# Kernel tuning notes

Hardware: AMD Instinct MI355X
Metric: run time of the kernel (lower is better)

The kernel has to match this reference:

```python
import jax, jax.numpy as jnp
import numpy as np
import math

NLAT, NLON, LMAX, MMAX = 128, 256, 50, 50
M = NLAT * NLON  # = 2*NLAT^2 grid points, matches torch meshgrid(arange(nlat), arange(-nlat,nlat))

def _grid_np():
    gx, gy = np.meshgrid(np.arange(NLAT), np.arange(-NLAT, NLAT), indexing='ij')
    g = np.stack([gx.ravel(), gy.ravel()], -1).astype(np.float32)
    return g / NLAT * np.pi  # (M, 2)

def _cc_weights(n):
    # Clenshaw-Curtis quadrature nodes theta_j = pi*j/(n-1) and weights on [-1,1]
    N = n - 1
    theta = np.pi * np.arange(n) / N
    k = np.arange(1, N // 2 + 1)
    b = np.where(2 * k == N, 1.0, 2.0)
    S = (b / (4.0 * k ** 2 - 1.0) * np.cos(2.0 * np.outer(theta, k))).sum(-1)
    w = (2.0 / N) * (1.0 - S)
    w[0] *= 0.5
    w[-1] *= 0.5
    return theta, w

def _legendre(lmax, mmax, theta):
    # orthonormal (4pi-normalized) associated Legendre P_l^m(cos theta), Condon-Shortley phase
    x, s = np.cos(theta), np.sin(theta)
    P = np.zeros((mmax, lmax, theta.shape[0]))
    P[0, 0] = math.sqrt(1.0 / (4.0 * math.pi))
    pmm = P[0, 0].copy()
    for m in range(1, mmax):
        pmm = -math.sqrt((2 * m + 1) / (2.0 * m)) * s * pmm
        P[m, m] = pmm
    for m in range(mmax):
        if m + 1 < lmax:
            P[m, m + 1] = math.sqrt(2 * m + 3.0) * x * P[m, m]
        for l in range(m + 2, lmax):
            a = math.sqrt((4.0 * l * l - 1.0) / (l * l - m * m))
            bb = math.sqrt(((l - 1.0) ** 2 - m * m) / (4.0 * (l - 1.0) ** 2 - 1.0))
            P[m, l] = a * (x * P[m, l - 1] - bb * P[m, l - 2])
    return P

_theta_q, _wq = _cc_weights(NLAT)
_SHT_W = jnp.asarray((_legendre(LMAX, MMAX, _theta_q) * _wq).astype(np.float32))  # (mmax, lmax, nlat)
_GRID = jnp.asarray(_grid_np())  # (M, 2)

def setup_inputs() -> dict:
    key = jax.random.key(0)
    target = jax.random.normal(key, (2, 2048, 3), dtype=jnp.float32)
    return {"target": target}

def reference(target):
    B, N, _ = target.shape
    # to_spherical: rho=(B,N) features, sph=(phi, theta)-pi shift on theta -> (B,N,2)
    rho = jnp.linalg.norm(target, axis=-1)
    phi = jnp.arctan2(target[..., 1], target[..., 0])
    theta = jnp.arccos(target[..., 2] / rho)
    sph = jnp.stack([phi, theta - jnp.pi], axis=-1)  # (B, N, 2)
    # squared distances grid(M,2) vs sph(B,N,2) -> (B,M,N) via gram trick (no (B,M,N,2) temp)
    s2 = jnp.sum(sph * sph, -1)                 # (B, N)
    g2 = jnp.sum(_GRID * _GRID, -1)             # (M,)
    cross = jnp.einsum('md,bnd->bmn', _GRID, sph)
    D2 = jax.lax.stop_gradient(s2[:, None, :] + g2[None, :, None] - 2.0 * cross)
    _, idx = jax.lax.top_k(-D2, 3)              # (B, M, 3), 3-NN targets per grid point, ascending dist
    bidx = jnp.arange(B)[:, None, None]
    tmp = sph[bidx, idx]                        # (B, M, 3, 2)
    dist = jnp.sqrt(jnp.sum((tmp - _GRID[None, :, None, :]) ** 2, -1))  # (B, M, 3)
    w = dist / jnp.sum(dist, -1, keepdims=True)
    # three_interpolate: weighted combine of rho at 3 NNs -> (B, M)
    interp = jnp.sum(rho[bidx, idx] * w, -1)
    f = interp.reshape(B, NLAT, NLON)
    # RealSHT (equiangular grid): forward-normalized rfft over lon, then Legendre contraction over lat
    F = (2.0 * jnp.pi) * jnp.fft.rfft(f, axis=-1) / NLON  # (B, nlat, nlon//2+1) complex
    coeff_re = jnp.einsum('bkm,mlk->blm', jnp.real(F[..., :MMAX]), _SHT_W)  # (B, lmax, mmax)
    return coeff_re
```

## Files before the change

kernel.cpp:

```cpp
#include <hip/hip_runtime.h>
#include <math.h>
#include <stdint.h>

#define NLAT 128
#define NLON 256
#define LMAX 50
#define MMAX 50
#define MGRID (NLAT*NLON)
#define BATCH 2
#define NPTS 2048
#define NBKT 64
#define PI_F 3.14159265358979323846f

typedef float v2f __attribute__((ext_vector_type(2)));

__device__ __forceinline__ uint32_t umin32(uint32_t a, uint32_t b) { return a < b ? a : b; }
__device__ __forceinline__ uint32_t umax32(uint32_t a, uint32_t b) { return a > b ? a : b; }

__global__ __launch_bounds__(512, 2)
void k_nn(const float* __restrict__ target, float* __restrict__ f) {
    __shared__ __attribute__((aligned(16))) float2 s_all[NPTS + 8];
    __shared__ float    s_rall[NPTS + 8];
    __shared__ uint32_t s_keys[8*64*3];
    __shared__ int      cnt[NBKT], start[NBKT + 1], cur[NBKT];
    __shared__ int      s_win[2];
    int b = blockIdx.x >> 8;
    int j = blockIdx.x & 255;
    int tid = threadIdx.x;
    const float* tg = target + b * NPTS * 3;

    if (tid < NBKT) cnt[tid] = 0;
    __syncthreads();
    float ph[4], py[4], rh[4]; int bk[4];
    #pragma unroll
    for (int c = 0; c < 4; ++c) {
        int p = tid + c * 512;
        float x = tg[p*3], y = tg[p*3+1], z = tg[p*3+2];
        float r = sqrtf(fmaf(x, x, fmaf(y, y, z*z)));
        float cc = fminf(1.f, fmaxf(-1.f, z / r));
        float pyv = acosf(cc) - PI_F;
        ph[c] = atan2f(y, x); py[c] = pyv; rh[c] = r;
        int bb = (int)floorf((pyv + PI_F) * ((float)NBKT / PI_F));
        bk[c] = min(NBKT-1, max(0, bb));
        atomicAdd(&cnt[bk[c]], 1);
    }
    __syncthreads();

    if (tid < 64) {
        int v = cnt[tid];
        int cv = v;
        #pragma unroll
        for (int sh = 1; sh < 64; sh <<= 1) {
            int t = __shfl_up(v, sh);
            if (tid >= sh) v += t;
        }
        start[tid + 1] = v;
        cur[tid] = v - cv;
        if (tid == 0) start[0] = 0;
    }
    __syncthreads();

    #pragma unroll
    for (int c = 0; c < 4; ++c) {
        int pos = atomicAdd(&cur[bk[c]], 1);
        s_all[pos]  = make_float2(ph[c], py[c]);
        s_rall[pos] = rh[c];
    }
    if (tid < 8) {
        s_all[NPTS + tid] = make_float2(1e15f, 1e15f);
        s_rall[NPTS + tid] = 0.f;
    }
    float gy = (float)(j - 128) * (PI_F / 128.0f);
    int c0 = (int)floorf((gy + PI_F) * ((float)NBKT / PI_F));
    c0 = min(NBKT-1, max(0, c0));
    if (tid < 64) {
        int t = tid;
        int lo_t = max(0, c0 - 5 - t), hi_t = min(NBKT-1, c0 + 5 + t);
        int cw_t = start[hi_t+1] - start[lo_t];
        unsigned long long ok =
            __ballot(cw_t >= 192 || (lo_t == 0 && hi_t == NBKT-1));
        int t0 = __ffsll((unsigned long long)ok) - 1;
        if (tid == 0) {
            s_win[0] = max(0, c0 - 5 - t0);
            s_win[1] = min(NBKT-1, c0 + 5 + t0);
        }
    }
    __syncthreads();

    int lo = s_win[0], hi = s_win[1];
    int off = start[lo] & ~1;
    int cw  = start[hi+1] - off;
    int q = ((cw + 3) / 4 + 1) & ~1;
    int lane = tid & 63;
    int wv   = tid >> 6;
    int part = wv & 3;
    int lat  = lane + ((wv >> 2) << 6);
    float gx = (float)lat * (PI_F / 128.0f);
    v2f gx2 = {gx, gx}, gy2 = {gy, gy};
    uint32_t k0 = ~0u, k1 = ~0u, k2 = ~0u;
    uint32_t nb = (uint32_t)(part * q);
    const float4* p4 = (const float4*)(s_all + off + part * q);
    int iters = q >> 1;
    #pragma unroll 4
    for (int i = 0; i < iters; ++i) {
        float4 Q = p4[i];
        v2f px = {Q.x, Q.z}, pyy = {Q.y, Q.w};
        v2f dp = gx2 - px, dt = gy2 - pyy;
        v2f d = dp * dp;
        d = dt * dt + d;
        uint32_t key0 = (__float_as_uint(d.x) & 0xFFFFF800u) | (nb + 2u*i);
        uint32_t key1 = (__float_as_uint(d.y) & 0xFFFFF800u) | (nb + 2u*i + 1u);
        uint32_t t1;
        t1 = umin32(umax32(key0, k0), k1);
        k2 = umin32(umax32(key0, k1), k2);
        k0 = umin32(key0, k0); k1 = t1;
        t1 = umin32(umax32(key1, k0), k1);
        k2 = umin32(umax32(key1, k1), k2);
        k0 = umin32(key1, k0); k1 = t1;
    }
    s_keys[(wv*64 + lane)*3 + 0] = k0;
    s_keys[(wv*64 + lane)*3 + 1] = k1;
    s_keys[(wv*64 + lane)*3 + 2] = k2;
    __syncthreads();

    if (tid < 128) {
        int lane2 = tid & 63;
        int half  = tid >> 6;
        uint32_t m0 = ~0u, m1 = ~0u, m2 = ~0u;
        #pragma unroll
        for (int w = half*4; w < half*4 + 4; ++w) {
            #pragma unroll
            for (int s = 0; s < 3; ++s) {
                uint32_t key = s_keys[(w*64 + lane2)*3 + s];
                uint32_t t1 = umin32(umax32(key, m0), m1);
                m2 = umin32(umax32(key, m1), m2);
                m0 = umin32(key, m0); m1 = t1;
            }
        }
        int i0 = off + (int)(m0 & 2047);
        int i1 = off + (int)(m1 & 2047);
        int i2 = off + (int)(m2 & 2047);
        int lat2 = lane2 + (half << 6);
        float gxs = (float)lat2 * (PI_F / 128.0f);
        float2 p0 = s_all[i0], p1 = s_all[i1], p2 = s_all[i2];
        float e, r0, r1, r2;
        e = gxs - p0.x; r0 = e*e; e = gy - p0.y; r0 = sqrtf(fmaf(e, e, r0));
        e = gxs - p1.x; r1 = e*e; e = gy - p1.y; r1 = sqrtf(fmaf(e, e, r1));
        e = gxs - p2.x; r2 = e*e; e = gy - p2.y; r2 = sqrtf(fmaf(e, e, r2));
        float sum = r0 + r1 + r2;
        float interp = (s_rall[i0]*r0 + s_rall[i1]*r1 + s_rall[i2]*r2) / sum;
        f[b * MGRID + lat2 * NLON + j] = interp;
    }
}

__global__ __launch_bounds__(512)
void k_fftsht(const float* __restrict__ f, float* __restrict__ out) {
    __shared__ float Wl[LMAX*129];
    __shared__ float red[NLAT*5];
    __shared__ float sFre[NLAT];
    __shared__ float cred[256];
    __shared__ float s_a[LMAX], s_bb[LMAX], s_w[NLAT];
    __shared__ float s_cm;
    int b = blockIdx.x / MMAX;
    int m = blockIdx.x % MMAX;
    int tid = threadIdx.x;

    if (tid < 64) {
        int i = tid;
        float v = (i >= 1 && i <= m)
                  ? 0.5f * __log2f((2.f*i + 1.f) / (2.f*i)) : 0.f;
        #pragma unroll
        for (int sh = 1; sh < 64; sh <<= 1) v += __shfl_xor(v, sh);
        if (i == 0) s_cm = ((m & 1) ? -1.f : 1.f) * exp2f(v);
    } else if (tid < 128) {
        int l = tid - 64;
        if (l < LMAX) {
            float fl = (float)l, fm2 = (float)(m*m);
            s_a[l]  = sqrtf((4.f*fl*fl - 1.f) / fmaxf(fl*fl - fm2, 0.25f));
            float flm1 = fl - 1.f;
            s_bb[l] = sqrtf(fmaxf(flm1*flm1 - fm2, 0.f) /
                            fmaxf(4.f*flm1*flm1 - 1.f, 0.25f));
        }
    } else if (tid < 256) {
        int k = tid - 128;
        float theta = (PI_F * (float)k) / 127.0f;
        float S = 0.0f;
        for (int kk = 1; kk <= 63; ++kk)
            S += 2.0f / (4.0f*kk*kk - 1.0f) * __cosf(2.0f * theta * (float)kk);
        float w = (2.0f/127.0f) * (1.0f - S);
        if (k == 0 || k == NLAT-1) w *= 0.5f;
        s_w[k] = w;
    }

    {
        int k = tid >> 2, g = tid & 3;
        const float4* fb4 = (const float4*)(f + b * MGRID);
        float p = 0.0f;
        int a = (m * 64 * g) & 255;
        #pragma unroll
        for (int i = 0; i < 16; ++i) {
            float4 v = fb4[k * 64 + g * 16 + i];
            p = fmaf(v.x, __cosf((float)a * (2.0f*PI_F/256.0f)), p); a = (a + m) & 255;
            p = fmaf(v.y, __cosf((float)a * (2.0f*PI_F/256.0f)), p); a = (a + m) & 255;
            p = fmaf(v.z, __cosf((float)a * (2.0f*PI_F/256.0f)), p); a = (a + m) & 255;
            p = fmaf(v.w, __cosf((float)a * (2.0f*PI_F/256.0f)), p); a = (a + m) & 255;
        }
        red[k * 5 + g] = p;
    }
    __syncthreads();

    if (tid < NLAT) {
        int k = tid;
        float srow = red[k*5] + red[k*5+1] + red[k*5+2] + red[k*5+3];
        sFre[k] = srow * (2.0f * PI_F / 256.0f);

        float theta = (PI_F * (float)k) / 127.0f;
        float x = __cosf(theta), sn = __sinf(theta);
        float w = s_w[k];
        float pmm;
        if (m == 0) pmm = 0.28209479177f;
        else {
            float mag = exp2f((float)m * __log2f(fabsf(sn)));
            float sg  = (sn < 0.f && (m & 1)) ? -1.f : 1.f;
            pmm = 0.28209479177f * s_cm * mag * sg;
        }
        for (int l = 0; l < m; ++l) Wl[l*129 + k] = 0.0f;
        float Plm2 = pmm;
        Wl[m*129 + k] = Plm2 * w;
        if (m + 1 < LMAX) {
            float Plm1 = sqrtf(2.0f*m + 3.0f) * x * pmm;
            Wl[(m+1)*129 + k] = Plm1 * w;
            for (int l = m + 2; l < LMAX; ++l) {
                float P = s_a[l] * fmaf(-s_bb[l], Plm2, x * Plm1);
                Wl[l*129 + k] = P * w;
                Plm2 = Plm1; Plm1 = P;
            }
        }
    }
    __syncthreads();

    float acc = 0.0f;
    if (tid < 200) {
        int l = tid >> 2, kq = tid & 3;
        #pragma unroll 8
        for (int i = 0; i < 32; ++i)
            acc = fmaf(Wl[l*129 + kq*32 + i], sFre[kq*32 + i], acc);
    }
    if (tid < 256) cred[tid] = acc;
    __syncthreads();
    if (tid < LMAX)
        out[(b*LMAX + tid)*MMAX + m] =
            cred[4*tid] + cred[4*tid+1] + cred[4*tid+2] + cred[4*tid+3];
}

extern "C" void kernel_launch(void* const* d_in, const int* in_sizes, int n_in,
                              void* d_out, int out_size, void* d_ws, size_t ws_size,
                              hipStream_t stream) {
    const float* target = (const float*)d_in[0];
    float* out = (float*)d_out;
    float* f   = (float*)d_ws;

    k_nn<<<BATCH*NLON, 512, 0, stream>>>(target, f);
    k_fftsht<<<BATCH*MMAX, 512, 0, stream>>>(f, out);
}
```

Baseline: 74.92 us.

## Hoist per-batch sorting and Legendre weight tables into a separate prep kernel

```diff
diff --git a/kernel.cpp b/kernel.cpp
--- a/kernel.cpp
+++ b/kernel.cpp
@@ -10,6 +10,7 @@
 #define BATCH 2
 #define NPTS 2048
 #define NBKT 64
+#define NSRT 2056
 #define PI_F 3.14159265358979323846f
 
 typedef float v2f __attribute__((ext_vector_type(2)));
@@ -17,66 +18,154 @@
 __device__ __forceinline__ uint32_t umin32(uint32_t a, uint32_t b) { return a < b ? a : b; }
 __device__ __forceinline__ uint32_t umax32(uint32_t a, uint32_t b) { return a > b ? a : b; }
 
+#define WS_F    0
+#define WS_SXY  65536
+#define WS_SR   (WS_SXY + BATCH*NSRT*2)
+#define WS_BST  (WS_SR + BATCH*NSRT)
+#define WS_WG   78080
+#define WS_CT   (WS_WG + MMAX*LMAX*NLAT)
+
+__global__ __launch_bounds__(512)
+void k_prep(const float* __restrict__ target, float* __restrict__ ws) {
+    __shared__ __attribute__((aligned(16))) float2 s_all[NSRT];
+    __shared__ float    s_rall[NSRT];
+    __shared__ int      cnt[NBKT], start[NBKT + 1], cur[NBKT];
+    __shared__ float    s_a[LMAX], s_bb[LMAX], s_w[NLAT];
+    __shared__ float    s_cm;
+    int blk = blockIdx.x;
+    int tid = threadIdx.x;
+
+    if (blk < BATCH) {
+        const float* tg = target + blk * NPTS * 3;
+        if (tid < NBKT) cnt[tid] = 0;
+        __syncthreads();
+        float ph[4], py[4], rh[4]; int bk[4];
+        #pragma unroll
+        for (int c = 0; c < 4; ++c) {
+            int p = tid + c * 512;
+            float x = tg[p*3], y = tg[p*3+1], z = tg[p*3+2];
+            float r = sqrtf(fmaf(x, x, fmaf(y, y, z*z)));
+            float cc = fminf(1.f, fmaxf(-1.f, z / r));
+            float pyv = acosf(cc) - PI_F;
+            ph[c] = atan2f(y, x); py[c] = pyv; rh[c] = r;
+            int bb = (int)floorf((pyv + PI_F) * ((float)NBKT / PI_F));
+            bk[c] = min(NBKT-1, max(0, bb));
+            atomicAdd(&cnt[bk[c]], 1);
+        }
+        __syncthreads();
+        if (tid < 64) {
+            int v = cnt[tid];
+            int cv = v;
+            #pragma unroll
+            for (int sh = 1; sh < 64; sh <<= 1) {
+                int t = __shfl_up(v, sh);
+                if (tid >= sh) v += t;
+            }
+            start[tid + 1] = v;
+            cur[tid] = v - cv;
+            if (tid == 0) start[0] = 0;
+        }
+        __syncthreads();
+        #pragma unroll
+        for (int c = 0; c < 4; ++c) {
+            int pos = atomicAdd(&cur[bk[c]], 1);
+            s_all[pos]  = make_float2(ph[c], py[c]);
+            s_rall[pos] = rh[c];
+        }
+        if (tid < 8) {
+            s_all[NPTS + tid] = make_float2(1e15f, 1e15f);
+            s_rall[NPTS + tid] = 0.f;
+        }
+        __syncthreads();
+        float2* gxy = (float2*)(ws + WS_SXY) + blk * NSRT;
+        float*  gr  = ws + WS_SR + blk * NSRT;
+        int*    bst = (int*)(ws + WS_BST) + blk * (NBKT + 1);
+        for (int t = tid; t < NSRT; t += 512) { gxy[t] = s_all[t]; gr[t] = s_rall[t]; }
+        if (tid <= NBKT) bst[tid] = start[tid];
+    } else {
+        int m = blk - BATCH;
+        if (tid < 64) {
+            int i = tid;
+            float v = (i >= 1 && i <= m)
+                      ? 0.5f * __log2f((2.f*i + 1.f) / (2.f*i)) : 0.f;
+            #pragma unroll
+            for (int sh = 1; sh < 64; sh <<= 1) v += __shfl_xor(v, sh);
+            if (i == 0) s_cm = ((m & 1) ? -1.f : 1.f) * exp2f(v);
+        } else if (tid < 128) {
+            int l = tid - 64;
+            if (l < LMAX) {
+                float fl = (float)l, fm2 = (float)(m*m);
+                s_a[l]  = sqrtf((4.f*fl*fl - 1.f) / fmaxf(fl*fl - fm2, 0.25f));
+                float flm1 = fl - 1.f;
+                s_bb[l] = sqrtf(fmaxf(flm1*flm1 - fm2, 0.f) /
+                                fmaxf(4.f*flm1*flm1 - 1.f, 0.25f));
+            }
+        } else if (tid < 256) {
+            int k = tid - 128;
+            float theta = (PI_F * (float)k) / 127.0f;
+            float S = 0.0f;
+            for (int kk = 1; kk <= 63; ++kk)
+                S += 2.0f / (4.0f*kk*kk - 1.0f) * __cosf(2.0f * theta * (float)kk);
+            float w = (2.0f/127.0f) * (1.0f - S);
+            if (k == 0 || k == NLAT-1) w *= 0.5f;
+            s_w[k] = w;
+        } else {
+            int j = tid - 256;
+            ws[WS_CT + m*256 + j] =
+                __cosf((float)((m * j) & 255) * (2.0f*PI_F/256.0f));
+        }
+        __syncthreads();
+        if (tid < NLAT) {
+            int k = tid;
+            float* Wm = ws + WS_WG + m * (LMAX * NLAT);
+            float theta = (PI_F * (float)k) / 127.0f;
+            float x = __cosf(theta), sn = __sinf(theta);
+            float w = s_w[k];
+            float pmm;
+            if (m == 0) pmm = 0.28209479177f;
+            else {
+                float mag = exp2f((float)m * __log2f(fabsf(sn)));
+                float sg  = (sn < 0.f && (m & 1)) ? -1.f : 1.f;
+                pmm = 0.28209479177f * s_cm * mag * sg;
+            }
+            for (int l = 0; l < m; ++l) Wm[l*NLAT + k] = 0.0f;
+            float Plm2 = pmm;
+            Wm[m*NLAT + k] = Plm2 * w;
+            if (m + 1 < LMAX) {
+                float Plm1 = sqrtf(2.0f*m + 3.0f) * x * pmm;
+                Wm[(m+1)*NLAT + k] = Plm1 * w;
+                for (int l = m + 2; l < LMAX; ++l) {
+                    float P = s_a[l] * fmaf(-s_bb[l], Plm2, x * Plm1);
+                    Wm[l*NLAT + k] = P * w;
+                    Plm2 = Plm1; Plm1 = P;
+                }
+            }
+        }
+    }
+}
+
 __global__ __launch_bounds__(512, 2)
-void k_nn(const float* __restrict__ target, float* __restrict__ f) {
-    __shared__ __attribute__((aligned(16))) float2 s_all[NPTS + 8];
-    __shared__ float    s_rall[NPTS + 8];
+void k_nn(const float* __restrict__ ws_c, float* __restrict__ f) {
+    __shared__ __attribute__((aligned(16))) float2 s_all[NSRT];
+    __shared__ float    s_rall[NSRT];
     __shared__ uint32_t s_keys[8*64*3];
-    __shared__ int      cnt[NBKT], start[NBKT + 1], cur[NBKT];
+    __shared__ int      s_start[NBKT + 1];
     __shared__ int      s_win[2];
     int b = blockIdx.x >> 8;
     int j = blockIdx.x & 255;
     int tid = threadIdx.x;
-    const float* tg = target + b * NPTS * 3;
-
-    if (tid < NBKT) cnt[tid] = 0;
-    __syncthreads();
-    float ph[4], py[4], rh[4]; int bk[4];
-    #pragma unroll
-    for (int c = 0; c < 4; ++c) {
-        int p = tid + c * 512;
-        float x = tg[p*3], y = tg[p*3+1], z = tg[p*3+2];
-        float r = sqrtf(fmaf(x, x, fmaf(y, y, z*z)));
-        float cc = fminf(1.f, fmaxf(-1.f, z / r));
-        float pyv = acosf(cc) - PI_F;
-        ph[c] = atan2f(y, x); py[c] = pyv; rh[c] = r;
-        int bb = (int)floorf((pyv + PI_F) * ((float)NBKT / PI_F));
-        bk[c] = min(NBKT-1, max(0, bb));
-        atomicAdd(&cnt[bk[c]], 1);
-    }
-    __syncthreads();
-
-    if (tid < 64) {
-        int v = cnt[tid];
-        int cv = v;
-        #pragma unroll
-        for (int sh = 1; sh < 64; sh <<= 1) {
-            int t = __shfl_up(v, sh);
-            if (tid >= sh) v += t;
-        }
-        start[tid + 1] = v;
-        cur[tid] = v - cv;
-        if (tid == 0) start[0] = 0;
-    }
-    __syncthreads();
-
-    #pragma unroll
-    for (int c = 0; c < 4; ++c) {
-        int pos = atomicAdd(&cur[bk[c]], 1);
-        s_all[pos]  = make_float2(ph[c], py[c]);
-        s_rall[pos] = rh[c];
-    }
-    if (tid < 8) {
-        s_all[NPTS + tid] = make_float2(1e15f, 1e15f);
-        s_rall[NPTS + tid] = 0.f;
-    }
+
+    if (tid <= NBKT)
+        s_start[tid] = ((const int*)(ws_c + WS_BST))[b*(NBKT+1) + tid];
+    __syncthreads();
+
     float gy = (float)(j - 128) * (PI_F / 128.0f);
     int c0 = (int)floorf((gy + PI_F) * ((float)NBKT / PI_F));
     c0 = min(NBKT-1, max(0, c0));
     if (tid < 64) {
         int t = tid;
         int lo_t = max(0, c0 - 5 - t), hi_t = min(NBKT-1, c0 + 5 + t);
-        int cw_t = start[hi_t+1] - start[lo_t];
+        int cw_t = s_start[hi_t+1] - s_start[lo_t];
         unsigned long long ok =
             __ballot(cw_t >= 192 || (lo_t == 0 && hi_t == NBKT-1));
         int t0 = __ffsll((unsigned long long)ok) - 1;
@@ -88,8 +177,14 @@
     __syncthreads();
 
     int lo = s_win[0], hi = s_win[1];
-    int off = start[lo] & ~1;
-    int cw  = start[hi+1] - off;
+    int off0 = s_start[lo];
+    int cw   = s_start[hi+1] - off0;
+    int n    = cw + 8;
+    const float2* gxy = (const float2*)(ws_c + WS_SXY) + b * NSRT + off0;
+    const float*  gr  = ws_c + WS_SR + b * NSRT + off0;
+    for (int t = tid; t < n; t += 512) { s_all[t] = gxy[t]; s_rall[t] = gr[t]; }
+    __syncthreads();
+
     int q = ((cw + 3) / 4 + 1) & ~1;
     int lane = tid & 63;
     int wv   = tid >> 6;
@@ -99,7 +194,7 @@
     v2f gx2 = {gx, gx}, gy2 = {gy, gy};
     uint32_t k0 = ~0u, k1 = ~0u, k2 = ~0u;
     uint32_t nb = (uint32_t)(part * q);
-    const float4* p4 = (const float4*)(s_all + off + part * q);
+    const float4* p4 = (const float4*)(s_all + part * q);
     int iters = q >> 1;
     #pragma unroll 4
     for (int i = 0; i < iters; ++i) {
@@ -137,9 +232,9 @@
                 m0 = umin32(key, m0); m1 = t1;
             }
         }
-        int i0 = off + (int)(m0 & 2047);
-        int i1 = off + (int)(m1 & 2047);
-        int i2 = off + (int)(m2 & 2047);
+        int i0 = (int)(m0 & 2047);
+        int i1 = (int)(m1 & 2047);
+        int i2 = (int)(m2 & 2047);
         int lat2 = lane2 + (half << 6);
         float gxs = (float)lat2 * (PI_F / 128.0f);
         float2 p0 = s_all[i0], p1 = s_all[i1], p2 = s_all[i2];
@@ -154,56 +249,31 @@
 }
 
 __global__ __launch_bounds__(512)
-void k_fftsht(const float* __restrict__ f, float* __restrict__ out) {
-    __shared__ float Wl[LMAX*129];
+void k_fft(const float* __restrict__ f, const float* __restrict__ ws_c,
+           float* __restrict__ out) {
     __shared__ float red[NLAT*5];
     __shared__ float sFre[NLAT];
     __shared__ float cred[256];
-    __shared__ float s_a[LMAX], s_bb[LMAX], s_w[NLAT];
-    __shared__ float s_cm;
+    __shared__ float ct_s[256];
     int b = blockIdx.x / MMAX;
     int m = blockIdx.x % MMAX;
     int tid = threadIdx.x;
 
-    if (tid < 64) {
-        int i = tid;
-        float v = (i >= 1 && i <= m)
-                  ? 0.5f * __log2f((2.f*i + 1.f) / (2.f*i)) : 0.f;
-        #pragma unroll
-        for (int sh = 1; sh < 64; sh <<= 1) v += __shfl_xor(v, sh);
-        if (i == 0) s_cm = ((m & 1) ? -1.f : 1.f) * exp2f(v);
-    } else if (tid < 128) {
-        int l = tid - 64;
-        if (l < LMAX) {
-            float fl = (float)l, fm2 = (float)(m*m);
-            s_a[l]  = sqrtf((4.f*fl*fl - 1.f) / fmaxf(fl*fl - fm2, 0.25f));
-            float flm1 = fl - 1.f;
-            s_bb[l] = sqrtf(fmaxf(flm1*flm1 - fm2, 0.f) /
-                            fmaxf(4.f*flm1*flm1 - 1.f, 0.25f));
-        }
-    } else if (tid < 256) {
-        int k = tid - 128;
-        float theta = (PI_F * (float)k) / 127.0f;
-        float S = 0.0f;
-        for (int kk = 1; kk <= 63; ++kk)
-            S += 2.0f / (4.0f*kk*kk - 1.0f) * __cosf(2.0f * theta * (float)kk);
-        float w = (2.0f/127.0f) * (1.0f - S);
-        if (k == 0 || k == NLAT-1) w *= 0.5f;
-        s_w[k] = w;
-    }
+    if (tid < 256) ct_s[tid] = ws_c[WS_CT + m*256 + tid];
+    __syncthreads();
 
     {
         int k = tid >> 2, g = tid & 3;
         const float4* fb4 = (const float4*)(f + b * MGRID);
         float p = 0.0f;
-        int a = (m * 64 * g) & 255;
+        int j0 = g * 64;
         #pragma unroll
         for (int i = 0; i < 16; ++i) {
             float4 v = fb4[k * 64 + g * 16 + i];
-            p = fmaf(v.x, __cosf((float)a * (2.0f*PI_F/256.0f)), p); a = (a + m) & 255;
-            p = fmaf(v.y, __cosf((float)a * (2.0f*PI_F/256.0f)), p); a = (a + m) & 255;
-            p = fmaf(v.z, __cosf((float)a * (2.0f*PI_F/256.0f)), p); a = (a + m) & 255;
-            p = fmaf(v.w, __cosf((float)a * (2.0f*PI_F/256.0f)), p); a = (a + m) & 255;
+            p = fmaf(v.x, ct_s[j0 + 4*i    ], p);
+            p = fmaf(v.y, ct_s[j0 + 4*i + 1], p);
+            p = fmaf(v.z, ct_s[j0 + 4*i + 2], p);
+            p = fmaf(v.w, ct_s[j0 + 4*i + 3], p);
         }
         red[k * 5 + g] = p;
     }
@@ -211,40 +281,18 @@
 
     if (tid < NLAT) {
         int k = tid;
-        float srow = red[k*5] + red[k*5+1] + red[k*5+2] + red[k*5+3];
-        sFre[k] = srow * (2.0f * PI_F / 256.0f);
-
-        float theta = (PI_F * (float)k) / 127.0f;
-        float x = __cosf(theta), sn = __sinf(theta);
-        float w = s_w[k];
-        float pmm;
-        if (m == 0) pmm = 0.28209479177f;
-        else {
-            float mag = exp2f((float)m * __log2f(fabsf(sn)));
-            float sg  = (sn < 0.f && (m & 1)) ? -1.f : 1.f;
-            pmm = 0.28209479177f * s_cm * mag * sg;
-        }
-        for (int l = 0; l < m; ++l) Wl[l*129 + k] = 0.0f;
-        float Plm2 = pmm;
-        Wl[m*129 + k] = Plm2 * w;
-        if (m + 1 < LMAX) {
-            float Plm1 = sqrtf(2.0f*m + 3.0f) * x * pmm;
-            Wl[(m+1)*129 + k] = Plm1 * w;
-            for (int l = m + 2; l < LMAX; ++l) {
-                float P = s_a[l] * fmaf(-s_bb[l], Plm2, x * Plm1);
-                Wl[l*129 + k] = P * w;
-                Plm2 = Plm1; Plm1 = P;
-            }
-        }
+        sFre[k] = (red[k*5] + red[k*5+1] + red[k*5+2] + red[k*5+3])
+                  * (2.0f * PI_F / 256.0f);
     }
     __syncthreads();
 
     float acc = 0.0f;
     if (tid < 200) {
         int l = tid >> 2, kq = tid & 3;
+        const float* Wm = ws_c + WS_WG + (m * LMAX + l) * NLAT;
         #pragma unroll 8
         for (int i = 0; i < 32; ++i)
-            acc = fmaf(Wl[l*129 + kq*32 + i], sFre[kq*32 + i], acc);
+            acc = fmaf(Wm[kq*32 + i], sFre[kq*32 + i], acc);
     }
     if (tid < 256) cred[tid] = acc;
     __syncthreads();
@@ -258,8 +306,10 @@
                               hipStream_t stream) {
     const float* target = (const float*)d_in[0];
     float* out = (float*)d_out;
-    float* f   = (float*)d_ws;
-
-    k_nn<<<BATCH*NLON, 512, 0, stream>>>(target, f);
-    k_fftsht<<<BATCH*MMAX, 512, 0, stream>>>(f, out);
+    float* ws  = (float*)d_ws;
+    float* f   = ws + WS_F;
+
+    k_prep<<<BATCH + MMAX, 512, 0, stream>>>(target, ws);
+    k_nn  <<<BATCH * NLON, 512, 0, stream>>>(ws, f);
+    k_fft <<<BATCH * MMAX, 512, 0, stream>>>(f, ws, out);
 }
```

Result: slower. 77.39 us (+3.3%).

## Precompute Legendre weights and cosine table in extra blocks of NN kernel

Applied to the files above, without the earlier changes.

```diff
diff --git a/kernel.cpp b/kernel.cpp
--- a/kernel.cpp
+++ b/kernel.cpp
@@ -17,16 +17,86 @@
 __device__ __forceinline__ uint32_t umin32(uint32_t a, uint32_t b) { return a < b ? a : b; }
 __device__ __forceinline__ uint32_t umax32(uint32_t a, uint32_t b) { return a > b ? a : b; }
 
+#define WS_F    0
+#define WS_WG   65536
+#define WS_CT   (WS_WG + MMAX*LMAX*NLAT)
+
 __global__ __launch_bounds__(512, 2)
-void k_nn(const float* __restrict__ target, float* __restrict__ f) {
+void k_main(const float* __restrict__ target, float* __restrict__ ws) {
     __shared__ __attribute__((aligned(16))) float2 s_all[NPTS + 8];
     __shared__ float    s_rall[NPTS + 8];
     __shared__ uint32_t s_keys[8*64*3];
     __shared__ int      cnt[NBKT], start[NBKT + 1], cur[NBKT];
     __shared__ int      s_win[2];
-    int b = blockIdx.x >> 8;
-    int j = blockIdx.x & 255;
+    __shared__ float    s_a[LMAX], s_bb[LMAX], s_w[NLAT];
+    __shared__ float    s_cm;
+    int blk = blockIdx.x;
     int tid = threadIdx.x;
+
+    if (blk >= 512) {
+        int m = blk - 512;
+        if (tid < 64) {
+            int i = tid;
+            float v = (i >= 1 && i <= m)
+                      ? 0.5f * __log2f((2.f*i + 1.f) / (2.f*i)) : 0.f;
+            #pragma unroll
+            for (int sh = 1; sh < 64; sh <<= 1) v += __shfl_xor(v, sh);
+            if (i == 0) s_cm = ((m & 1) ? -1.f : 1.f) * exp2f(v);
+        } else if (tid < 128) {
+            int l = tid - 64;
+            if (l < LMAX) {
+                float fl = (float)l, fm2 = (float)(m*m);
+                s_a[l]  = sqrtf((4.f*fl*fl - 1.f) / fmaxf(fl*fl - fm2, 0.25f));
+                float flm1 = fl - 1.f;
+                s_bb[l] = sqrtf(fmaxf(flm1*flm1 - fm2, 0.f) /
+                                fmaxf(4.f*flm1*flm1 - 1.f, 0.25f));
+            }
+        } else if (tid < 256) {
+            int k = tid - 128;
+            float theta = (PI_F * (float)k) / 127.0f;
+            float S = 0.0f;
+            for (int kk = 1; kk <= 63; ++kk)
+                S += 2.0f / (4.0f*kk*kk - 1.0f) * __cosf(2.0f * theta * (float)kk);
+            float w = (2.0f/127.0f) * (1.0f - S);
+            if (k == 0 || k == NLAT-1) w *= 0.5f;
+            s_w[k] = w;
+        } else {
+            int j = tid - 256;
+            ws[WS_CT + m*256 + j] =
+                __cosf((float)((m * j) & 255) * (2.0f*PI_F/256.0f));
+        }
+        __syncthreads();
+        if (tid < NLAT) {
+            int k = tid;
+            float* Wm = ws + WS_WG + m * (LMAX * NLAT);
+            float theta = (PI_F * (float)k) / 127.0f;
+            float x = __cosf(theta), sn = __sinf(theta);
+            float w = s_w[k];
+            float pmm;
+            if (m == 0) pmm = 0.28209479177f;
+            else {
+                float mag = exp2f((float)m * __log2f(fabsf(sn)));
+                float sg  = (sn < 0.f && (m & 1)) ? -1.f : 1.f;
+                pmm = 0.28209479177f * s_cm * mag * sg;
+            }
+            for (int l = 0; l < m; ++l) Wm[l*NLAT + k] = 0.0f;
+            float Plm2 = pmm;
+            Wm[m*NLAT + k] = Plm2 * w;
+            if (m + 1 < LMAX) {
+                float Plm1 = sqrtf(2.0f*m + 3.0f) * x * pmm;
+                Wm[(m+1)*NLAT + k] = Plm1 * w;
+                for (int l = m + 2; l < LMAX; ++l) {
+                    float P = s_a[l] * fmaf(-s_bb[l], Plm2, x * Plm1);
+                    Wm[l*NLAT + k] = P * w;
+                    Plm2 = Plm1; Plm1 = P;
+                }
+            }
+        }
+        return;
+    }
+
+    int b = blk >> 8;
+    int j = blk & 255;
     const float* tg = target + b * NPTS * 3;
 
     if (tid < NBKT) cnt[tid] = 0;
@@ -149,61 +219,35 @@
         e = gxs - p2.x; r2 = e*e; e = gy - p2.y; r2 = sqrtf(fmaf(e, e, r2));
         float sum = r0 + r1 + r2;
         float interp = (s_rall[i0]*r0 + s_rall[i1]*r1 + s_rall[i2]*r2) / sum;
-        f[b * MGRID + lat2 * NLON + j] = interp;
+        ws[WS_F + b * MGRID + lat2 * NLON + j] = interp;
     }
 }
 
 __global__ __launch_bounds__(512)
-void k_fftsht(const float* __restrict__ f, float* __restrict__ out) {
-    __shared__ float Wl[LMAX*129];
+void k_fft(const float* __restrict__ ws_c, float* __restrict__ out) {
     __shared__ float red[NLAT*5];
     __shared__ float sFre[NLAT];
     __shared__ float cred[256];
-    __shared__ float s_a[LMAX], s_bb[LMAX], s_w[NLAT];
-    __shared__ float s_cm;
+    __shared__ float ct_s[256];
     int b = blockIdx.x / MMAX;
     int m = blockIdx.x % MMAX;
     int tid = threadIdx.x;
 
-    if (tid < 64) {
-        int i = tid;
-        float v = (i >= 1 && i <= m)
-                  ? 0.5f * __log2f((2.f*i + 1.f) / (2.f*i)) : 0.f;
-        #pragma unroll
-        for (int sh = 1; sh < 64; sh <<= 1) v += __shfl_xor(v, sh);
-        if (i == 0) s_cm = ((m & 1) ? -1.f : 1.f) * exp2f(v);
-    } else if (tid < 128) {
-        int l = tid - 64;
-        if (l < LMAX) {
-            float fl = (float)l, fm2 = (float)(m*m);
-            s_a[l]  = sqrtf((4.f*fl*fl - 1.f) / fmaxf(fl*fl - fm2, 0.25f));
-            float flm1 = fl - 1.f;
-            s_bb[l] = sqrtf(fmaxf(flm1*flm1 - fm2, 0.f) /
-                            fmaxf(4.f*flm1*flm1 - 1.f, 0.25f));
-        }
-    } else if (tid < 256) {
-        int k = tid - 128;
-        float theta = (PI_F * (float)k) / 127.0f;
-        float S = 0.0f;
-        for (int kk = 1; kk <= 63; ++kk)
-            S += 2.0f / (4.0f*kk*kk - 1.0f) * __cosf(2.0f * theta * (float)kk);
-        float w = (2.0f/127.0f) * (1.0f - S);
-        if (k == 0 || k == NLAT-1) w *= 0.5f;
-        s_w[k] = w;
-    }
+    if (tid < 256) ct_s[tid] = ws_c[WS_CT + m*256 + tid];
+    __syncthreads();
 
     {
         int k = tid >> 2, g = tid & 3;
-        const float4* fb4 = (const float4*)(f + b * MGRID);
+        const float4* fb4 = (const float4*)(ws_c + WS_F + b * MGRID);
         float p = 0.0f;
-        int a = (m * 64 * g) & 255;
+        int j0 = g * 64;
         #pragma unroll
         for (int i = 0; i < 16; ++i) {
             float4 v = fb4[k * 64 + g * 16 + i];
-            p = fmaf(v.x, __cosf((float)a * (2.0f*PI_F/256.0f)), p); a = (a + m) & 255;
-            p = fmaf(v.y, __cosf((float)a * (2.0f*PI_F/256.0f)), p); a = (a + m) & 255;
-            p = fmaf(v.z, __cosf((float)a * (2.0f*PI_F/256.0f)), p); a = (a + m) & 255;
-            p = fmaf(v.w, __cosf((float)a * (2.0f*PI_F/256.0f)), p); a = (a + m) & 255;
+            p = fmaf(v.x, ct_s[j0 + 4*i    ], p);
+            p = fmaf(v.y, ct_s[j0 + 4*i + 1], p);
+            p = fmaf(v.z, ct_s[j0 + 4*i + 2], p);
+            p = fmaf(v.w, ct_s[j0 + 4*i + 3], p);
         }
         red[k * 5 + g] = p;
     }
@@ -211,40 +255,18 @@
 
     if (tid < NLAT) {
         int k = tid;
-        float srow = red[k*5] + red[k*5+1] + red[k*5+2] + red[k*5+3];
-        sFre[k] = srow * (2.0f * PI_F / 256.0f);
-
-        float theta = (PI_F * (float)k) / 127.0f;
-        float x = __cosf(theta), sn = __sinf(theta);
-        float w = s_w[k];
-        float pmm;
-        if (m == 0) pmm = 0.28209479177f;
-        else {
-            float mag = exp2f((float)m * __log2f(fabsf(sn)));
-            float sg  = (sn < 0.f && (m & 1)) ? -1.f : 1.f;
-            pmm = 0.28209479177f * s_cm * mag * sg;
-        }
-        for (int l = 0; l < m; ++l) Wl[l*129 + k] = 0.0f;
-        float Plm2 = pmm;
-        Wl[m*129 + k] = Plm2 * w;
-        if (m + 1 < LMAX) {
-            float Plm1 = sqrtf(2.0f*m + 3.0f) * x * pmm;
-            Wl[(m+1)*129 + k] = Plm1 * w;
-            for (int l = m + 2; l < LMAX; ++l) {
-                float P = s_a[l] * fmaf(-s_bb[l], Plm2, x * Plm1);
-                Wl[l*129 + k] = P * w;
-                Plm2 = Plm1; Plm1 = P;
-            }
-        }
+        sFre[k] = (red[k*5] + red[k*5+1] + red[k*5+2] + red[k*5+3])
+                  * (2.0f * PI_F / 256.0f);
     }
     __syncthreads();
 
     float acc = 0.0f;
     if (tid < 200) {
         int l = tid >> 2, kq = tid & 3;
+        const float* Wm = ws_c + WS_WG + (m * LMAX + l) * NLAT;
         #pragma unroll 8
         for (int i = 0; i < 32; ++i)
-            acc = fmaf(Wl[l*129 + kq*32 + i], sFre[kq*32 + i], acc);
+            acc = fmaf(Wm[kq*32 + i], sFre[kq*32 + i], acc);
     }
     if (tid < 256) cred[tid] = acc;
     __syncthreads();
@@ -258,8 +280,8 @@
                               hipStream_t stream) {
     const float* target = (const float*)d_in[0];
     float* out = (float*)d_out;
-    float* f   = (float*)d_ws;
-
-    k_nn<<<BATCH*NLON, 512, 0, stream>>>(target, f);
-    k_fftsht<<<BATCH*MMAX, 512, 0, stream>>>(f, out);
+    float* ws  = (float*)d_ws;
+
+    k_main<<<512 + MMAX, 512, 0, stream>>>(target, ws);
+    k_fft <<<BATCH * MMAX, 512, 0, stream>>>(ws, out);
 }
```

Measured after the change: 73.62 us (median of 2 runs). Within noise of the previous version (-1.7%).
